# Performance work log

Measured on AMD Instinct MI355X. Metric: run time of the kernel, lower is better.

The kernel has to match this reference:

```python
import jax, jax.numpy as jnp
import numpy as np

D = 1024          # label_size / in_features
V = 100000        # vocab size
SHORTLIST = 10000 # cutoffs[0]
# tail clusters: (proj_dim, cluster_size) per div_value=2 schedule
TAILS = [(512, 10000), (256, 20000), (128, 40000), (64, 20000)]


def setup_inputs() -> dict:
    key = jax.random.key(0)
    ks = jax.random.split(key, 11)
    s = jnp.float32(0.02)
    inp = {
        "feature": jax.random.normal(ks[0], (D,), jnp.float32),
        "targets": jax.random.randint(ks[1], (4096,), 0, V),
        "head_w": jax.random.normal(ks[2], (SHORTLIST + len(TAILS), D), jnp.float32) * s,
    }
    for i, (h, c) in enumerate(TAILS):
        inp[f"t{i}p"] = jax.random.normal(ks[3 + 2 * i], (h, D), jnp.float32) * s
        inp[f"t{i}w"] = jax.random.normal(ks[4 + 2 * i], (c, h), jnp.float32) * s
    return inp


def reference(feature, targets, head_w, t0p, t0w, t1p, t1w, t2p, t2w, t3p, t3w):
    # head logits: [SHORTLIST + n_clusters]
    head_lp = jax.nn.log_softmax(head_w @ feature)
    parts = [head_lp[:SHORTLIST]]
    tails = [(t0p, t0w), (t1p, t1w), (t2p, t2w), (t3p, t3w)]
    for i, (p, w) in enumerate(tails):
        # two-stage low-rank projection: [h] then cluster logits [c]
        cl_lp = jax.nn.log_softmax(w @ (p @ feature)) + head_lp[SHORTLIST + i]
        parts.append(cl_lp)
    logprob = jnp.concatenate(parts)  # [V] full-vocab log-probabilities
    return -jnp.mean(logprob[targets])
```

## Files before the change

kernel.cpp:

```cpp
#include <hip/hip_runtime.h>
#include <math.h>

#define NHEAD     10004
#define OFF_HEAD  0
#define OFF_H0    10004
#define OFF_H1    10516
#define OFF_H2    10772
#define OFF_H3    10900
#define OFF_C0    10964
#define OFF_C1    20964
#define OFF_C2    40964
#define OFF_C3    80964
#define OFF_PH    100964
#define OFF_P0    101590
#define OFF_P1    102215
#define OFF_P2    102840
#define OFF_P3    104090
#define OFF_G     104403

__device__ __forceinline__ float wave_sum(float v) {
  v += __shfl_xor(v, 32, 64);
  v += __shfl_xor(v, 16, 64);
  v += __shfl_xor(v, 8, 64);
  v += __shfl_xor(v, 4, 64);
  v += __shfl_xor(v, 2, 64);
  v += __shfl_xor(v, 1, 64);
  return v;
}

__global__ __launch_bounds__(256) void head_proj_kernel(
    const float* __restrict__ feat, const float* __restrict__ head_w,
    const float* __restrict__ p0, const float* __restrict__ p1,
    const float* __restrict__ p2, const float* __restrict__ p3,
    float* __restrict__ ws) {
  __shared__ __align__(16) float sf[1024];
  ((float4*)sf)[threadIdx.x] = ((const float4*)feat)[threadIdx.x];
  __syncthreads();
  const float4* sf4 = (const float4*)sf;
  const int wave = threadIdx.x >> 6, lane = threadIdx.x & 63;
  const int b = blockIdx.x;

  if (b < 626) {
    float esum = 0.f;
#pragma unroll
    for (int k = 0; k < 4; ++k) {
      int row = b * 16 + wave * 4 + k;
      if (row < NHEAD) {
        const float4* src4 = (const float4*)head_w + (size_t)row * 256;
        float acc = 0.f;
#pragma unroll
        for (int j = 0; j < 4; ++j) {
          float4 a = src4[lane + j * 64];
          float4 c = sf4[lane + j * 64];
          acc += a.x * c.x + a.y * c.y + a.z * c.z + a.w * c.w;
        }
        acc = wave_sum(acc);
        if (lane == 0) { ws[OFF_HEAD + row] = acc; esum += expf(acc); }
      }
    }
    __shared__ float wred[4];
    if (lane == 0) wred[wave] = esum;
    __syncthreads();
    if (threadIdx.x == 0) ws[OFF_PH + b] = wred[0] + wred[1] + wred[2] + wred[3];
  } else {
    const int pb = b - 626;
#pragma unroll
    for (int k = 0; k < 4; ++k) {
      int row = NHEAD + pb * 16 + wave * 4 + k;
      const float* src;
      if (row < 10516)      src = p0 + (size_t)(row - 10004) * 1024;
      else if (row < 10772) src = p1 + (size_t)(row - 10516) * 1024;
      else if (row < 10900) src = p2 + (size_t)(row - 10772) * 1024;
      else                  src = p3 + (size_t)(row - 10900) * 1024;
      const float4* src4 = (const float4*)src;
      float acc = 0.f;
#pragma unroll
      for (int j = 0; j < 4; ++j) {
        float4 a = src4[lane + j * 64];
        float4 c = sf4[lane + j * 64];
        acc += a.x * c.x + a.y * c.y + a.z * c.z + a.w * c.w;
      }
      acc = wave_sum(acc);
      if (lane == 0) ws[row] = acc;
    }
  }
}

__global__ __launch_bounds__(256) void tail_kernel(
    const float* __restrict__ w0, const float* __restrict__ w1,
    const float* __restrict__ w2, const float* __restrict__ w3,
    float* __restrict__ ws) {
  __shared__ __align__(16) float sh[512];
  __shared__ float wred[4];
  const int b = blockIdx.x;
  const int wave = threadIdx.x >> 6, lane = threadIdx.x & 63;
  float esum = 0.f;
  int poff, lb;

  if (b < 625) {
    lb = b; poff = OFF_P0;
    for (int t = threadIdx.x; t < 512; t += 256) sh[t] = ws[OFF_H0 + t];
    __syncthreads();
    const float4* sh4 = (const float4*)sh;
    const int row0 = lb * 16 + wave * 4;
#pragma unroll
    for (int k = 0; k < 4; ++k) {
      const float4* wr4 = (const float4*)(w0 + (size_t)(row0 + k) * 512);
      float acc = 0.f;
#pragma unroll
      for (int j = 0; j < 2; ++j) {
        float4 a = wr4[lane + j * 64]; float4 c = sh4[lane + j * 64];
        acc += a.x * c.x + a.y * c.y + a.z * c.z + a.w * c.w;
      }
      acc = wave_sum(acc);
      if (lane == 0) { ws[OFF_C0 + row0 + k] = acc; esum += expf(acc); }
    }
  } else if (b < 1250) {
    lb = b - 625; poff = OFF_P1;
    if (threadIdx.x < 256) sh[threadIdx.x] = ws[OFF_H1 + threadIdx.x];
    __syncthreads();
    const float4 c = ((const float4*)sh)[lane];
    const int row0 = lb * 32 + wave * 8;
#pragma unroll
    for (int k = 0; k < 8; ++k) {
      float4 a = ((const float4*)(w1 + (size_t)(row0 + k) * 256))[lane];
      float acc = a.x * c.x + a.y * c.y + a.z * c.z + a.w * c.w;
      acc = wave_sum(acc);
      if (lane == 0) { ws[OFF_C1 + row0 + k] = acc; esum += expf(acc); }
    }
  } else if (b < 2500) {
    lb = b - 1250; poff = OFF_P2;
    if (threadIdx.x < 128) sh[threadIdx.x] = ws[OFF_H2 + threadIdx.x];
    __syncthreads();
    const float2 c = ((const float2*)sh)[lane];
    const int row0 = lb * 32 + wave * 8;
#pragma unroll
    for (int k = 0; k < 8; ++k) {
      float2 a = ((const float2*)(w2 + (size_t)(row0 + k) * 128))[lane];
      float acc = a.x * c.x + a.y * c.y;
      acc = wave_sum(acc);
      if (lane == 0) { ws[OFF_C2 + row0 + k] = acc; esum += expf(acc); }
    }
  } else {
    lb = b - 2500; poff = OFF_P3;
    if (threadIdx.x < 64) sh[threadIdx.x] = ws[OFF_H3 + threadIdx.x];
    __syncthreads();
    const float c = sh[lane];
    const int row0 = lb * 64 + wave * 16;
#pragma unroll
    for (int k = 0; k < 16; ++k) {
      int row = row0 + k;
      int rc = min(row, 19999);
      float a = w3[(size_t)rc * 64 + lane];
      float acc = wave_sum(a * c);
      if (lane == 0 && row < 20000) { ws[OFF_C3 + row] = acc; esum += expf(acc); }
    }
  }
  if (lane == 0) wred[wave] = esum;
  __syncthreads();
  if (threadIdx.x == 0) ws[poff + lb] = wred[0] + wred[1] + wred[2] + wred[3];
}

__global__ __launch_bounds__(256) void gather_kernel(
    const int* __restrict__ targets, float* __restrict__ ws) {
  __shared__ float red[256];
  __shared__ float slse[5];
  const int offs[5] = {OFF_PH, OFF_P0, OFF_P1, OFF_P2, OFF_P3};
  const int lens[5] = {626, 625, 625, 1250, 313};
  for (int s = 0; s < 5; ++s) {
    float v = 0.f;
    for (int i = threadIdx.x; i < lens[s]; i += 256) v += ws[offs[s] + i];
    red[threadIdx.x] = v; __syncthreads();
    for (int st = 128; st; st >>= 1) {
      if (threadIdx.x < st) red[threadIdx.x] += red[threadIdx.x + st];
      __syncthreads();
    }
    if (threadIdx.x == 0) slse[s] = logf(red[0]);
    __syncthreads();
  }
  const float lse0 = slse[0], lse1 = slse[1], lse2 = slse[2], lse3 = slse[3], lse4 = slse[4];
  const int i = blockIdx.x * 256 + threadIdx.x;
  const int t = targets[i];
  float lp;
  if (t < 10000)      lp = ws[OFF_HEAD + t] - lse0;
  else if (t < 20000) lp = ws[OFF_C0 + t - 10000] - lse1 + (ws[10000] - lse0);
  else if (t < 40000) lp = ws[OFF_C1 + t - 20000] - lse2 + (ws[10001] - lse0);
  else if (t < 80000) lp = ws[OFF_C2 + t - 40000] - lse3 + (ws[10002] - lse0);
  else                lp = ws[OFF_C3 + t - 80000] - lse4 + (ws[10003] - lse0);
  float s = wave_sum(lp);
  __shared__ float wred[4];
  const int wave = threadIdx.x >> 6, lane = threadIdx.x & 63;
  if (lane == 0) wred[wave] = s;
  __syncthreads();
  if (threadIdx.x == 0) ws[OFF_G + blockIdx.x] = wred[0] + wred[1] + wred[2] + wred[3];
}

__global__ __launch_bounds__(64) void writeout_kernel(
    const float* __restrict__ ws, float* __restrict__ out) {
  float v = (threadIdx.x < 16) ? ws[OFF_G + threadIdx.x] : 0.f;
  v = wave_sum(v);
  if (threadIdx.x == 0) out[0] = -v * (1.f / 4096.f);
}

extern "C" void kernel_launch(void* const* d_in, const int* in_sizes, int n_in,
                              void* d_out, int out_size, void* d_ws, size_t ws_size,
                              hipStream_t stream) {
  const float* feat    = (const float*)d_in[0];
  const int*   targets = (const int*)d_in[1];
  const float* head_w  = (const float*)d_in[2];
  const float* t0p = (const float*)d_in[3];
  const float* t0w = (const float*)d_in[4];
  const float* t1p = (const float*)d_in[5];
  const float* t1w = (const float*)d_in[6];
  const float* t2p = (const float*)d_in[7];
  const float* t2w = (const float*)d_in[8];
  const float* t3p = (const float*)d_in[9];
  const float* t3w = (const float*)d_in[10];
  float* ws  = (float*)d_ws;
  float* out = (float*)d_out;

  head_proj_kernel<<<686, 256, 0, stream>>>(feat, head_w, t0p, t1p, t2p, t3p, ws);
  tail_kernel<<<2813, 256, 0, stream>>>(t0w, t1w, t2w, t3w, ws);
  gather_kernel<<<16, 256, 0, stream>>>(targets, ws);
  writeout_kernel<<<1, 64, 0, stream>>>(ws, out);
}
```

Baseline: 170.4 us.

## Merge gather and writeout kernels, double rows per tail block, pack short rows per wave

The gather and writeout kernels become a single 1024-thread finalize kernel that reduces all per-block partial sums in one pass and writes the mean directly, which drops one launch and the serial shared-memory reduction loops. The tail kernel now has each block handle twice as many rows (1564 blocks instead of 2813). For the 128- and 64-wide clusters, several rows are packed into one wave with float4 loads and a partial shuffle reduction, so fewer lanes sit idle. The cost is a single-block finalize stage with lower parallelism for the target gather, and more serial work per tail block.

```diff
diff --git a/kernel.cpp b/kernel.cpp
--- a/kernel.cpp
+++ b/kernel.cpp
@@ -11,12 +11,13 @@
 #define OFF_C1    20964
 #define OFF_C2    40964
 #define OFF_C3    80964
+#define OFF_P     100964
 #define OFF_PH    100964
 #define OFF_P0    101590
-#define OFF_P1    102215
-#define OFF_P2    102840
-#define OFF_P3    104090
-#define OFF_G     104403
+#define OFF_P1    101903
+#define OFF_P2    102216
+#define OFF_P3    102841
+#define NPART     2190
 
 __device__ __forceinline__ float wave_sum(float v) {
   v += __shfl_xor(v, 32, 64);
@@ -28,6 +29,10 @@
   return v;
 }
 
+__device__ __forceinline__ float dot4(float4 a, float4 c) {
+  return a.x * c.x + a.y * c.y + a.z * c.z + a.w * c.w;
+}
+
 __global__ __launch_bounds__(256) void head_proj_kernel(
     const float* __restrict__ feat, const float* __restrict__ head_w,
     const float* __restrict__ p0, const float* __restrict__ p1,
@@ -45,18 +50,13 @@
 #pragma unroll
     for (int k = 0; k < 4; ++k) {
       int row = b * 16 + wave * 4 + k;
-      if (row < NHEAD) {
-        const float4* src4 = (const float4*)head_w + (size_t)row * 256;
-        float acc = 0.f;
-#pragma unroll
-        for (int j = 0; j < 4; ++j) {
-          float4 a = src4[lane + j * 64];
-          float4 c = sf4[lane + j * 64];
-          acc += a.x * c.x + a.y * c.y + a.z * c.z + a.w * c.w;
-        }
-        acc = wave_sum(acc);
-        if (lane == 0) { ws[OFF_HEAD + row] = acc; esum += expf(acc); }
-      }
+      int rc = min(row, NHEAD - 1);
+      const float4* src4 = (const float4*)head_w + (size_t)rc * 256;
+      float acc = 0.f;
+#pragma unroll
+      for (int j = 0; j < 4; ++j) acc += dot4(src4[lane + j * 64], sf4[lane + j * 64]);
+      acc = wave_sum(acc);
+      if (lane == 0 && row < NHEAD) { ws[OFF_HEAD + row] = acc; esum += expf(acc); }
     }
     __shared__ float wred[4];
     if (lane == 0) wred[wave] = esum;
@@ -75,11 +75,7 @@
       const float4* src4 = (const float4*)src;
       float acc = 0.f;
 #pragma unroll
-      for (int j = 0; j < 4; ++j) {
-        float4 a = src4[lane + j * 64];
-        float4 c = sf4[lane + j * 64];
-        acc += a.x * c.x + a.y * c.y + a.z * c.z + a.w * c.w;
-      }
+      for (int j = 0; j < 4; ++j) acc += dot4(src4[lane + j * 64], sf4[lane + j * 64]);
       acc = wave_sum(acc);
       if (lane == 0) ws[row] = acc;
     }
@@ -97,109 +93,135 @@
   float esum = 0.f;
   int poff, lb;
 
-  if (b < 625) {
+  if (b < 313) {
     lb = b; poff = OFF_P0;
-    for (int t = threadIdx.x; t < 512; t += 256) sh[t] = ws[OFF_H0 + t];
+    if (threadIdx.x < 128) ((float4*)sh)[threadIdx.x] = ((const float4*)(ws + OFF_H0))[threadIdx.x];
     __syncthreads();
     const float4* sh4 = (const float4*)sh;
-    const int row0 = lb * 16 + wave * 4;
-#pragma unroll
-    for (int k = 0; k < 4; ++k) {
-      const float4* wr4 = (const float4*)(w0 + (size_t)(row0 + k) * 512);
-      float acc = 0.f;
-#pragma unroll
-      for (int j = 0; j < 2; ++j) {
-        float4 a = wr4[lane + j * 64]; float4 c = sh4[lane + j * 64];
-        acc += a.x * c.x + a.y * c.y + a.z * c.z + a.w * c.w;
+    const float4 cv0 = sh4[lane], cv1 = sh4[lane + 64];
+    const int row0 = lb * 32 + wave * 8;
+#pragma unroll
+    for (int k = 0; k < 8; ++k) {
+      int rc = min(row0 + k, 9999);
+      const float4* wr4 = (const float4*)(w0 + (size_t)rc * 512);
+      float acc = dot4(wr4[lane], cv0) + dot4(wr4[lane + 64], cv1);
+      acc = wave_sum(acc);
+      if (lane == 0 && row0 + k < 10000) { ws[OFF_C0 + row0 + k] = acc; esum += expf(acc); }
+    }
+  } else if (b < 626) {
+    lb = b - 313; poff = OFF_P1;
+    if (threadIdx.x < 64) ((float4*)sh)[threadIdx.x] = ((const float4*)(ws + OFF_H1))[threadIdx.x];
+    __syncthreads();
+    const float4 cv = ((const float4*)sh)[lane];
+    const int row0 = lb * 64 + wave * 16;
+#pragma unroll
+    for (int k = 0; k < 16; ++k) {
+      int rc = min(row0 + k, 19999);
+      float acc = dot4(((const float4*)(w1 + (size_t)rc * 256))[lane], cv);
+      acc = wave_sum(acc);
+      if (lane == 0 && row0 + k < 20000) { ws[OFF_C1 + row0 + k] = acc; esum += expf(acc); }
+    }
+  } else if (b < 1251) {
+    lb = b - 626; poff = OFF_P2;
+    if (threadIdx.x < 32) ((float4*)sh)[threadIdx.x] = ((const float4*)(ws + OFF_H2))[threadIdx.x];
+    __syncthreads();
+    const float4 cv = ((const float4*)sh)[lane & 31];
+    const int row0 = lb * 64 + wave * 16;
+#pragma unroll
+    for (int p = 0; p < 8; ++p) {
+      int rbase = row0 + 2 * p;
+      float acc = dot4(((const float4*)w2)[(size_t)rbase * 32 + lane], cv);
+      acc += __shfl_xor(acc, 1, 64);
+      acc += __shfl_xor(acc, 2, 64);
+      acc += __shfl_xor(acc, 4, 64);
+      acc += __shfl_xor(acc, 8, 64);
+      acc += __shfl_xor(acc, 16, 64);
+      if ((lane & 31) == 0) {
+        int r = rbase + (lane >> 5);
+        ws[OFF_C2 + r] = acc; esum += expf(acc);
       }
-      acc = wave_sum(acc);
-      if (lane == 0) { ws[OFF_C0 + row0 + k] = acc; esum += expf(acc); }
-    }
-  } else if (b < 1250) {
-    lb = b - 625; poff = OFF_P1;
-    if (threadIdx.x < 256) sh[threadIdx.x] = ws[OFF_H1 + threadIdx.x];
-    __syncthreads();
-    const float4 c = ((const float4*)sh)[lane];
-    const int row0 = lb * 32 + wave * 8;
-#pragma unroll
-    for (int k = 0; k < 8; ++k) {
-      float4 a = ((const float4*)(w1 + (size_t)(row0 + k) * 256))[lane];
-      float acc = a.x * c.x + a.y * c.y + a.z * c.z + a.w * c.w;
-      acc = wave_sum(acc);
-      if (lane == 0) { ws[OFF_C1 + row0 + k] = acc; esum += expf(acc); }
-    }
-  } else if (b < 2500) {
-    lb = b - 1250; poff = OFF_P2;
-    if (threadIdx.x < 128) sh[threadIdx.x] = ws[OFF_H2 + threadIdx.x];
-    __syncthreads();
-    const float2 c = ((const float2*)sh)[lane];
-    const int row0 = lb * 32 + wave * 8;
-#pragma unroll
-    for (int k = 0; k < 8; ++k) {
-      float2 a = ((const float2*)(w2 + (size_t)(row0 + k) * 128))[lane];
-      float acc = a.x * c.x + a.y * c.y;
-      acc = wave_sum(acc);
-      if (lane == 0) { ws[OFF_C2 + row0 + k] = acc; esum += expf(acc); }
     }
   } else {
-    lb = b - 2500; poff = OFF_P3;
-    if (threadIdx.x < 64) sh[threadIdx.x] = ws[OFF_H3 + threadIdx.x];
-    __syncthreads();
-    const float c = sh[lane];
+    lb = b - 1251; poff = OFF_P3;
+    if (threadIdx.x < 16) ((float4*)sh)[threadIdx.x] = ((const float4*)(ws + OFF_H3))[threadIdx.x];
+    __syncthreads();
+    const float4 cv = ((const float4*)sh)[lane & 15];
     const int row0 = lb * 64 + wave * 16;
 #pragma unroll
-    for (int k = 0; k < 16; ++k) {
-      int row = row0 + k;
-      int rc = min(row, 19999);
-      float a = w3[(size_t)rc * 64 + lane];
-      float acc = wave_sum(a * c);
-      if (lane == 0 && row < 20000) { ws[OFF_C3 + row] = acc; esum += expf(acc); }
-    }
-  }
+    for (int q = 0; q < 4; ++q) {
+      int rb = row0 + 4 * q;
+      int rbc = min(rb, 19996);
+      float acc = dot4(((const float4*)w3)[(size_t)rbc * 16 + lane], cv);
+      acc += __shfl_xor(acc, 1, 64);
+      acc += __shfl_xor(acc, 2, 64);
+      acc += __shfl_xor(acc, 4, 64);
+      acc += __shfl_xor(acc, 8, 64);
+      if ((lane & 15) == 0 && rb < 20000) {
+        int r = rb + (lane >> 4);
+        ws[OFF_C3 + r] = acc; esum += expf(acc);
+      }
+    }
+  }
+  esum = wave_sum(esum);
   if (lane == 0) wred[wave] = esum;
   __syncthreads();
   if (threadIdx.x == 0) ws[poff + lb] = wred[0] + wred[1] + wred[2] + wred[3];
 }
 
-__global__ __launch_bounds__(256) void gather_kernel(
-    const int* __restrict__ targets, float* __restrict__ ws) {
-  __shared__ float red[256];
+__global__ __launch_bounds__(1024) void finalize_kernel(
+    const int* __restrict__ targets, float* __restrict__ ws,
+    float* __restrict__ out) {
+  const int wv = threadIdx.x >> 6, lane = threadIdx.x & 63;
+  float a0 = 0.f, a1 = 0.f, a2 = 0.f, a3 = 0.f, a4 = 0.f;
+#pragma unroll
+  for (int it = 0; it < 3; ++it) {
+    int i = threadIdx.x + it * 1024;
+    if (i < NPART) {
+      float v = ws[OFF_P + i];
+      if (i < 626)       a0 += v;
+      else if (i < 939)  a1 += v;
+      else if (i < 1252) a2 += v;
+      else if (i < 1877) a3 += v;
+      else               a4 += v;
+    }
+  }
+  a0 = wave_sum(a0); a1 = wave_sum(a1); a2 = wave_sum(a2);
+  a3 = wave_sum(a3); a4 = wave_sum(a4);
+  __shared__ float r5[16][5];
   __shared__ float slse[5];
-  const int offs[5] = {OFF_PH, OFF_P0, OFF_P1, OFF_P2, OFF_P3};
-  const int lens[5] = {626, 625, 625, 1250, 313};
-  for (int s = 0; s < 5; ++s) {
-    float v = 0.f;
-    for (int i = threadIdx.x; i < lens[s]; i += 256) v += ws[offs[s] + i];
-    red[threadIdx.x] = v; __syncthreads();
-    for (int st = 128; st; st >>= 1) {
-      if (threadIdx.x < st) red[threadIdx.x] += red[threadIdx.x + st];
-      __syncthreads();
-    }
-    if (threadIdx.x == 0) slse[s] = logf(red[0]);
-    __syncthreads();
-  }
+  if (lane == 0) { r5[wv][0] = a0; r5[wv][1] = a1; r5[wv][2] = a2; r5[wv][3] = a3; r5[wv][4] = a4; }
+  __syncthreads();
+  if (threadIdx.x < 5) {
+    float s = 0.f;
+#pragma unroll
+    for (int w = 0; w < 16; ++w) s += r5[w][threadIdx.x];
+    slse[threadIdx.x] = logf(s);
+  }
+  __syncthreads();
   const float lse0 = slse[0], lse1 = slse[1], lse2 = slse[2], lse3 = slse[3], lse4 = slse[4];
-  const int i = blockIdx.x * 256 + threadIdx.x;
-  const int t = targets[i];
-  float lp;
-  if (t < 10000)      lp = ws[OFF_HEAD + t] - lse0;
-  else if (t < 20000) lp = ws[OFF_C0 + t - 10000] - lse1 + (ws[10000] - lse0);
-  else if (t < 40000) lp = ws[OFF_C1 + t - 20000] - lse2 + (ws[10001] - lse0);
-  else if (t < 80000) lp = ws[OFF_C2 + t - 40000] - lse3 + (ws[10002] - lse0);
-  else                lp = ws[OFF_C3 + t - 80000] - lse4 + (ws[10003] - lse0);
-  float s = wave_sum(lp);
-  __shared__ float wred[4];
-  const int wave = threadIdx.x >> 6, lane = threadIdx.x & 63;
-  if (lane == 0) wred[wave] = s;
-  __syncthreads();
-  if (threadIdx.x == 0) ws[OFF_G + blockIdx.x] = wred[0] + wred[1] + wred[2] + wred[3];
-}
-
-__global__ __launch_bounds__(64) void writeout_kernel(
-    const float* __restrict__ ws, float* __restrict__ out) {
-  float v = (threadIdx.x < 16) ? ws[OFF_G + threadIdx.x] : 0.f;
-  v = wave_sum(v);
-  if (threadIdx.x == 0) out[0] = -v * (1.f / 4096.f);
+  const float g0 = ws[10000] - lse0, g1 = ws[10001] - lse0;
+  const float g2 = ws[10002] - lse0, g3 = ws[10003] - lse0;
+  float s = 0.f;
+#pragma unroll
+  for (int it = 0; it < 4; ++it) {
+    int t = targets[threadIdx.x + it * 1024];
+    float lp;
+    if (t < 10000)      lp = ws[OFF_HEAD + t] - lse0;
+    else if (t < 20000) lp = ws[OFF_C0 + t - 10000] - lse1 + g0;
+    else if (t < 40000) lp = ws[OFF_C1 + t - 20000] - lse2 + g1;
+    else if (t < 80000) lp = ws[OFF_C2 + t - 40000] - lse3 + g2;
+    else                lp = ws[OFF_C3 + t - 80000] - lse4 + g3;
+    s += lp;
+  }
+  s = wave_sum(s);
+  if (lane == 0) r5[wv][0] = s;
+  __syncthreads();
+  if (threadIdx.x == 0) {
+    float tot = 0.f;
+#pragma unroll
+    for (int w = 0; w < 16; ++w) tot += r5[w][0];
+    out[0] = -tot * (1.f / 4096.f);
+  }
 }
 
 extern "C" void kernel_launch(void* const* d_in, const int* in_sizes, int n_in,
@@ -220,7 +242,6 @@
   float* out = (float*)d_out;
 
   head_proj_kernel<<<686, 256, 0, stream>>>(feat, head_w, t0p, t1p, t2p, t3p, ws);
-  tail_kernel<<<2813, 256, 0, stream>>>(t0w, t1w, t2w, t3w, ws);
-  gather_kernel<<<16, 256, 0, stream>>>(targets, ws);
-  writeout_kernel<<<1, 64, 0, stream>>>(ws, out);
-}
+  tail_kernel<<<1564, 256, 0, stream>>>(t0w, t1w, t2w, t3w, ws);
+  finalize_kernel<<<1, 1024, 0, stream>>>(targets, ws, out);
+}
```

Measured after the change: 164.6 us. 3.4% less time.
